# Optimization experiments

Measured on AMD Instinct MI355X. Metric: run time of the kernel, lower is better.

The kernel has to match this reference:

```python
import jax, jax.numpy as jnp
import numpy as np

N = 20000      # nodes
E = 320000     # edges (avg degree 16)
IN, HID, OUT, H = 128, 32, 32, 8
NEG_SLOPE = 0.2


def _gat_conv(x, src, dst, W, al, ar, b):
    """One DGL-style GATConv. x: [N, F_in], W: [F_in, H*D], al/ar: [H, D], b: [H*D].
    Returns [N, H, D]."""
    n = x.shape[0]
    Hh, D = al.shape
    feat = (x @ W).reshape(n, Hh, D)                      # [N,H,D]
    el = jnp.sum(feat * al[None], axis=-1)                # [N,H]
    er = jnp.sum(feat * ar[None], axis=-1)                # [N,H]
    e = jax.nn.leaky_relu(el[src] + er[dst], NEG_SLOPE)   # [E,H]
    # edge softmax over incoming edges of each dst node (stable)
    emax = jax.ops.segment_max(e, dst, num_segments=n)    # [N,H]
    ee = jnp.exp(e - emax[dst])                           # [E,H]
    denom = jax.ops.segment_sum(ee, dst, num_segments=n)  # [N,H]
    alpha = ee / denom[dst]                               # [E,H]
    msg = feat[src] * alpha[:, :, None]                   # [E,H,D] gather+weight
    out = jax.ops.segment_sum(msg, dst, num_segments=n)   # [N,H,D] scatter-add
    return out + b.reshape(1, Hh, D)


def setup_inputs() -> dict:
    key = jax.random.key(0)
    ks = jax.random.split(key, 11)
    return {
        "x":   jax.random.normal(ks[0], (N, IN), dtype=jnp.float32),
        "src": jax.random.randint(ks[1], (E,), 0, N, dtype=jnp.int32),
        "dst": jax.random.randint(ks[2], (E,), 0, N, dtype=jnp.int32),
        "W1":  jax.random.normal(ks[3], (IN, H * HID), dtype=jnp.float32) * 0.1,
        "al1": jax.random.normal(ks[4], (H, HID), dtype=jnp.float32) * 0.1,
        "ar1": jax.random.normal(ks[5], (H, HID), dtype=jnp.float32) * 0.1,
        "b1":  jnp.zeros((H * HID,), dtype=jnp.float32),
        "W2":  jax.random.normal(ks[6], (HID, H * OUT), dtype=jnp.float32) * 0.1,
        "al2": jax.random.normal(ks[7], (H, OUT), dtype=jnp.float32) * 0.1,
        "ar2": jax.random.normal(ks[8], (H, OUT), dtype=jnp.float32) * 0.1,
        "b2":  jnp.zeros((H * OUT,), dtype=jnp.float32),
    }


def reference(x, src, dst, W1, al1, ar1, b1, W2, al2, ar2, b2):
    h = _gat_conv(x, src, dst, W1, al1, ar1, b1)          # [N,H,HID]
    h = jnp.mean(jax.nn.relu(h), axis=1)                  # [N,HID]
    h = _gat_conv(h, src, dst, W2, al2, ar2, b2)          # [N,H,OUT]
    return jnp.mean(h, axis=1)                            # [N,OUT]
```

## Files before the change

kernel.cpp:

```cpp
#include <hip/hip_runtime.h>
#include <hip/hip_bf16.h>

#define N_NODES 20000
#define N_EDGES 320000
#define F_IN    128
#define F_HID   32
#define NHEAD   8
#define FDIM    256
#define CAP     96

typedef __hip_bfloat16 bf16;
typedef __attribute__((ext_vector_type(8))) short short8;
typedef __attribute__((ext_vector_type(4))) float f32x4;

__device__ __forceinline__ unsigned short f2bf_rne(float f){
  unsigned u = __float_as_uint(f);
  unsigned r = u + 0x7FFFu + ((u >> 16) & 1u);
  return (unsigned short)(r >> 16);
}
__device__ __forceinline__ float bf2f(unsigned short s){
  return __uint_as_float((unsigned)s << 16);
}

#define FILLB  ((N_EDGES + 255) / 256)
__global__ void prep_kernel(const int* __restrict__ src, const int* __restrict__ dst,
                            int* __restrict__ cnt, int* __restrict__ bucket,
                            const float* __restrict__ W1, const float* __restrict__ W2,
                            const float* __restrict__ al2, const float* __restrict__ ar2,
                            unsigned short* __restrict__ h1, unsigned short* __restrict__ l1,
                            float* __restrict__ q_lt, float* __restrict__ q_rt){
  const int b = blockIdx.x;
  if (b < FILLB){
    int i = b*256 + threadIdx.x;
    if (i < N_EDGES){
      int d = dst[i];
      int p = atomicAdd(&cnt[d], 1);
      if (p < CAP) bucket[(size_t)d*CAP + p] = src[i];
    }
  } else if (b < FILLB + 128){
    int i = (b - FILLB)*256 + threadIdx.x;
    int n = i >> 7, k = i & 127;
    float v = W1[(size_t)k*FDIM + n];
    unsigned short hs = f2bf_rne(v);
    h1[i] = hs;
    l1[i] = f2bf_rne(v - bf2f(hs));
  } else {
    int t = threadIdx.x;
    int k = t >> 3, hh = t & 7;
    float sl = 0.f, sr = 0.f;
    #pragma unroll
    for (int d = 0; d < 32; d++){
      float w = W2[(size_t)k*FDIM + hh*32 + d];
      sl = fmaf(w, al2[hh*32 + d], sl);
      sr = fmaf(w, ar2[hh*32 + d], sr);
    }
    q_lt[t] = sl;
    q_rt[t] = sr;
  }
}

template<int K>
__global__ __launch_bounds__(256) void gemm_mfma_kernel(
    const float* __restrict__ X,
    const unsigned short* __restrict__ Wthi, const unsigned short* __restrict__ Wtlo,
    const float* __restrict__ al, const float* __restrict__ ar,
    unsigned short* __restrict__ feat, float* __restrict__ el, float* __restrict__ er)
{
  const int tid  = threadIdx.x;
  const int wv   = tid >> 6;
  const int lane = tid & 63;
  const int quad = lane >> 4;
  const int l16  = lane & 15;
  const int m0   = blockIdx.x * 16;
  constexpr int NC = K / 32;

  short8 Ah[NC], Al_[NC];
  {
    const float* xrow = X + (size_t)(m0 + l16)*K;
    #pragma unroll
    for (int c = 0; c < NC; c++){
      float4 a0 = *(const float4*)(xrow + c*32 + quad*8);
      float4 a1 = *(const float4*)(xrow + c*32 + quad*8 + 4);
      const float vs[8] = {a0.x,a0.y,a0.z,a0.w,a1.x,a1.y,a1.z,a1.w};
      #pragma unroll
      for (int j = 0; j < 8; j++){
        unsigned short hs = f2bf_rne(vs[j]);
        Ah[c][j]  = (short)hs;
        Al_[c][j] = (short)f2bf_rne(vs[j] - bf2f(hs));
      }
    }
  }

  float elp[8], erp[8];
  #pragma unroll
  for (int j = 0; j < 8; j++){ elp[j] = 0.f; erp[j] = 0.f; }

  #pragma unroll
  for (int t = 0; t < 4; t++){
    const int nc = wv*64 + t*16;
    const size_t brow = (size_t)(nc + l16) * K;
    f32x4 acc = {0.f, 0.f, 0.f, 0.f};
    #pragma unroll
    for (int c = 0; c < NC; c++){
      short8 Bh = *(const short8*)(Wthi + brow + c*32 + quad*8);
      short8 Bl = *(const short8*)(Wtlo + brow + c*32 + quad*8);
      acc = __builtin_amdgcn_mfma_f32_16x16x32_bf16(Ah[c],  Bh, acc, 0, 0, 0);
      acc = __builtin_amdgcn_mfma_f32_16x16x32_bf16(Ah[c],  Bl, acc, 0, 0, 0);
      acc = __builtin_amdgcn_mfma_f32_16x16x32_bf16(Al_[c], Bh, acc, 0, 0, 0);
    }
    const float alv = al[nc + l16];
    const float arv = ar[nc + l16];
    const int hl = t >> 1;
    #pragma unroll
    for (int r = 0; r < 4; r++){
      float v = acc[r];
      feat[(size_t)(m0 + quad*4 + r)*FDIM + nc + l16] = f2bf_rne(v);
      elp[r*2 + hl] = fmaf(v, alv, elp[r*2 + hl]);
      erp[r*2 + hl] = fmaf(v, arv, erp[r*2 + hl]);
    }
  }

  #pragma unroll
  for (int off = 1; off <= 8; off <<= 1){
    #pragma unroll
    for (int j = 0; j < 8; j++){
      elp[j] += __shfl_xor(elp[j], off);
      erp[j] += __shfl_xor(erp[j], off);
    }
  }
  __shared__ float el_lds[16][8], er_lds[16][8];
  if (l16 == 0){
    #pragma unroll
    for (int r = 0; r < 4; r++){
      #pragma unroll
      for (int hl = 0; hl < 2; hl++){
        el_lds[quad*4 + r][wv*2 + hl] = elp[r*2 + hl];
        er_lds[quad*4 + r][wv*2 + hl] = erp[r*2 + hl];
      }
    }
  }
  __syncthreads();
  if (tid < 128){
    int row = tid >> 3, h = tid & 7;
    el[(size_t)(m0 + row)*NHEAD + h] = el_lds[row][h];
    er[(size_t)(m0 + row)*NHEAD + h] = er_lds[row][h];
  }
}

__global__ __launch_bounds__(256) void edge_agg_l1(
    const bf16* __restrict__ feat, const float* __restrict__ el,
    const float* __restrict__ er, const int* __restrict__ cnt,
    const int* __restrict__ bucket, const float* __restrict__ bias,
    const float* __restrict__ q_lt, const float* __restrict__ q_rt,
    unsigned short* __restrict__ h_out, float* __restrict__ el2,
    float* __restrict__ er2)
{
  const int tid  = threadIdx.x;
  const int wv   = tid >> 6;
  const int lane = tid & 63;
  const int n    = blockIdx.x*4 + wv;

  __shared__ float t_all[4][CAP*9];
  __shared__ int   s_all[4][CAP];
  __shared__ float sum_all[4][NHEAD];
  __shared__ float v_all[4][256];
  float* t_w = t_all[wv];
  int*   s_w = s_all[wv];

  int C = cnt[n];
  if (C > CAP) C = CAP;

  const float4* er4 = (const float4*)(er + (size_t)n*NHEAD);
  float4 era = er4[0], erb = er4[1];
  const float erv[8] = {era.x, era.y, era.z, era.w, erb.x, erb.y, erb.z, erb.w};

  for (int idx = lane; idx < C*2; idx += 64){
    const int e = idx >> 1, j = idx & 1;
    const int sidx = bucket[(size_t)n*CAP + e];
    if (j == 0) s_w[e] = sidx;
    float4 a = ((const float4*)(el + (size_t)sidx*NHEAD))[j];
    const float ev[4] = {a.x, a.y, a.z, a.w};
    #pragma unroll
    for (int hh = 0; hh < 4; hh++){
      float v = ev[hh] + erv[j*4 + hh];
      t_w[e*9 + j*4 + hh] = (v > 0.f) ? v : 0.2f*v;
    }
  }
  {
    const int h = lane >> 3, d = lane & 7;
    float lm = -INFINITY;
    for (int e = d; e < C; e += 8) lm = fmaxf(lm, t_w[e*9 + h]);
    #pragma unroll
    for (int off = 4; off >= 1; off >>= 1) lm = fmaxf(lm, __shfl_xor(lm, off));
    float ls = 0.f;
    for (int e = d; e < C; e += 8){
      float ex = __expf(t_w[e*9 + h] - lm);
      t_w[e*9 + h] = ex;
      ls += ex;
    }
    #pragma unroll
    for (int off = 4; off >= 1; off >>= 1) ls += __shfl_xor(ls, off);
    if (d == 0) sum_all[wv][h] = ls;
  }

  const int sub = lane >> 5;
  const int l   = lane & 31;
  const int hB  = l >> 2;
  const int coff = l << 3;
  float acc[8] = {0,0,0,0,0,0,0,0};
  int e = sub;
  float4 fv;
  if (e < C) fv = *(const float4*)(feat + (size_t)s_w[e]*FDIM + coff);
  while (e < C){
    const int en = e + 2;
    float4 fnext;
    if (en < C) fnext = *(const float4*)(feat + (size_t)s_w[en]*FDIM + coff);
    const float w = t_w[e*9 + hB];
    const unsigned* u = (const unsigned*)&fv;
    #pragma unroll
    for (int j = 0; j < 4; j++){
      float flo = __uint_as_float(u[j] << 16);
      float fhi = __uint_as_float(u[j] & 0xFFFF0000u);
      acc[2*j]   = fmaf(w, flo, acc[2*j]);
      acc[2*j+1] = fmaf(w, fhi, acc[2*j+1]);
    }
    fv = fnext;
    e = en;
  }
  #pragma unroll
  for (int j = 0; j < 8; j++) acc[j] += __shfl_xor(acc[j], 32);

  if (lane < 32){
    const float s = sum_all[wv][l >> 2];
    const float4* b4 = (const float4*)(bias + coff);
    float4 ba = b4[0], bb = b4[1];
    float bv[8] = {ba.x, ba.y, ba.z, ba.w, bb.x, bb.y, bb.z, bb.w};
    float v[8];
    #pragma unroll
    for (int j = 0; j < 8; j++){
      float val = (C > 0) ? (acc[j] / s) : 0.f;
      val += bv[j];
      val = fmaxf(val, 0.f);
      v[j] = val;
    }
    float4* v4 = (float4*)&v_all[wv][coff];
    v4[0] = make_float4(v[0], v[1], v[2], v[3]);
    v4[1] = make_float4(v[4], v[5], v[6], v[7]);
  }
  if (lane < 32){
    float hsum = 0.f;
    #pragma unroll
    for (int hh = 0; hh < 8; hh++) hsum += v_all[wv][hh*32 + lane];
    hsum *= 0.125f;
    h_out[(size_t)n*32 + lane] = f2bf_rne(hsum);

    float4 qa0 = ((const float4*)(q_lt + lane*8))[0];
    float4 qa1 = ((const float4*)(q_lt + lane*8))[1];
    float4 qb0 = ((const float4*)(q_rt + lane*8))[0];
    float4 qb1 = ((const float4*)(q_rt + lane*8))[1];
    float pl[8] = {hsum*qa0.x, hsum*qa0.y, hsum*qa0.z, hsum*qa0.w,
                   hsum*qa1.x, hsum*qa1.y, hsum*qa1.z, hsum*qa1.w};
    float pr[8] = {hsum*qb0.x, hsum*qb0.y, hsum*qb0.z, hsum*qb0.w,
                   hsum*qb1.x, hsum*qb1.y, hsum*qb1.z, hsum*qb1.w};
    #pragma unroll
    for (int off = 1; off <= 16; off <<= 1){
      #pragma unroll
      for (int j = 0; j < 8; j++){
        pl[j] += __shfl_xor(pl[j], off);
        pr[j] += __shfl_xor(pr[j], off);
      }
    }
    if (l == 0){
      #pragma unroll
      for (int j = 0; j < 8; j++){
        el2[(size_t)n*NHEAD + j] = pl[j];
        er2[(size_t)n*NHEAD + j] = pr[j];
      }
    }
  }
}

__global__ __launch_bounds__(256) void edge_agg_l2(
    const unsigned short* __restrict__ h_bf, const float* __restrict__ el2,
    const float* __restrict__ er2, const int* __restrict__ cnt,
    const int* __restrict__ bucket, const float* __restrict__ W2,
    const float* __restrict__ b2, float* __restrict__ outp)
{
  const int tid  = threadIdx.x;
  const int wv   = tid >> 6;
  const int lane = tid & 63;
  const int n    = blockIdx.x*4 + wv;

  __shared__ float t_all[4][CAP*9];
  __shared__ int   s_all[4][CAP];
  __shared__ float sum_all[4][NHEAD];
  __shared__ float A_lds[4][NHEAD][33];
  __shared__ float red[4][256];
  float* t_w = t_all[wv];
  int*   s_w = s_all[wv];

  int C = cnt[n];
  if (C > CAP) C = CAP;

  const float4* er4 = (const float4*)(er2 + (size_t)n*NHEAD);
  float4 era = er4[0], erb = er4[1];
  const float erv[8] = {era.x, era.y, era.z, era.w, erb.x, erb.y, erb.z, erb.w};

  for (int idx = lane; idx < C*2; idx += 64){
    const int e = idx >> 1, j = idx & 1;
    const int sidx = bucket[(size_t)n*CAP + e];
    if (j == 0) s_w[e] = sidx;
    float4 a = ((const float4*)(el2 + (size_t)sidx*NHEAD))[j];
    const float ev[4] = {a.x, a.y, a.z, a.w};
    #pragma unroll
    for (int hh = 0; hh < 4; hh++){
      float v = ev[hh] + erv[j*4 + hh];
      t_w[e*9 + j*4 + hh] = (v > 0.f) ? v : 0.2f*v;
    }
  }
  {
    const int h = lane >> 3, d = lane & 7;
    float lm = -INFINITY;
    for (int e = d; e < C; e += 8) lm = fmaxf(lm, t_w[e*9 + h]);
    #pragma unroll
    for (int off = 4; off >= 1; off >>= 1) lm = fmaxf(lm, __shfl_xor(lm, off));
    float ls = 0.f;
    for (int e = d; e < C; e += 8){
      float ex = __expf(t_w[e*9 + h] - lm);
      t_w[e*9 + h] = ex;
      ls += ex;
    }
    #pragma unroll
    for (int off = 4; off >= 1; off >>= 1) ls += __shfl_xor(ls, off);
    if (d == 0) sum_all[wv][h] = ls;
  }

  const int h  = lane & 7;
  const int dg = lane >> 3;
  float A0=0.f, A1=0.f, A2=0.f, A3=0.f;
  int e = 0;
  ushort4 hv;
  if (e < C) hv = *(const ushort4*)(h_bf + (size_t)s_w[e]*32 + dg*4);
  while (e < C){
    const int en = e + 1;
    ushort4 hnext;
    if (en < C) hnext = *(const ushort4*)(h_bf + (size_t)s_w[en]*32 + dg*4);
    const float w = t_w[e*9 + h];
    A0 = fmaf(w, bf2f(hv.x), A0);
    A1 = fmaf(w, bf2f(hv.y), A1);
    A2 = fmaf(w, bf2f(hv.z), A2);
    A3 = fmaf(w, bf2f(hv.w), A3);
    hv = hnext;
    e = en;
  }
  {
    const float s = sum_all[wv][h];
    const float inv = (C > 0) ? (1.f / s) : 0.f;
    A_lds[wv][h][dg*4 + 0] = A0 * inv;
    A_lds[wv][h][dg*4 + 1] = A1 * inv;
    A_lds[wv][h][dg*4 + 2] = A2 * inv;
    A_lds[wv][h][dg*4 + 3] = A3 * inv;
  }
  __syncthreads();

  {
    const int c  = tid;
    const int hc = c >> 5;
    float p0=0.f, p1=0.f, p2=0.f, p3=0.f;
    for (int k = 0; k < F_HID; k++){
      float w = W2[(size_t)k*FDIM + c];
      p0 = fmaf(A_lds[0][hc][k], w, p0);
      p1 = fmaf(A_lds[1][hc][k], w, p1);
      p2 = fmaf(A_lds[2][hc][k], w, p2);
      p3 = fmaf(A_lds[3][hc][k], w, p3);
    }
    red[0][c] = p0; red[1][c] = p1; red[2][c] = p2; red[3][c] = p3;
  }
  __syncthreads();
  if (tid < 128){
    const int nn = tid >> 5, d = tid & 31;
    float s = 0.f, bm = 0.f;
    #pragma unroll
    for (int hh = 0; hh < 8; hh++){
      s  += red[nn][hh*32 + d];
      bm += b2[hh*32 + d];
    }
    outp[(size_t)(blockIdx.x*4 + nn)*32 + d] = (s + bm) * 0.125f;
  }
}

extern "C" void kernel_launch(void* const* d_in, const int* in_sizes, int n_in,
                              void* d_out, int out_size, void* d_ws, size_t ws_size,
                              hipStream_t stream)
{
  const float* x   = (const float*)d_in[0];
  const int*   src = (const int*)  d_in[1];
  const int*   dst = (const int*)  d_in[2];
  const float* W1  = (const float*)d_in[3];
  const float* al1 = (const float*)d_in[4];
  const float* ar1 = (const float*)d_in[5];
  const float* b1  = (const float*)d_in[6];
  const float* W2  = (const float*)d_in[7];
  const float* al2 = (const float*)d_in[8];
  const float* ar2 = (const float*)d_in[9];
  const float* b2  = (const float*)d_in[10];
  (void)in_sizes; (void)n_in; (void)out_size; (void)ws_size;

  size_t o = 0;
  char* base = (char*)d_ws;
  auto take = [&](size_t bytes) -> char* {
    char* p = base + o;
    o += (bytes + 255) & ~(size_t)255;
    return p;
  };
  unsigned short* feat  = (unsigned short*)take((size_t)N_NODES*FDIM*2);
  float* el1    = (float*)take((size_t)N_NODES*NHEAD*4);
  float* er1    = (float*)take((size_t)N_NODES*NHEAD*4);
  float* el2    = (float*)take((size_t)N_NODES*NHEAD*4);
  float* er2    = (float*)take((size_t)N_NODES*NHEAD*4);
  int*   cnt    = (int*)  take((size_t)N_NODES*4);
  int*   bucket = (int*)  take((size_t)N_NODES*CAP*4);
  unsigned short* hbf  = (unsigned short*)take((size_t)N_NODES*F_HID*2);
  unsigned short* W1th = (unsigned short*)take((size_t)FDIM*F_IN*2);
  unsigned short* W1tl = (unsigned short*)take((size_t)FDIM*F_IN*2);
  float* q_lt   = (float*)take((size_t)F_HID*NHEAD*4);
  float* q_rt   = (float*)take((size_t)F_HID*NHEAD*4);

  hipMemsetAsync(cnt, 0, (size_t)N_NODES*4, stream);
  prep_kernel<<<FILLB + 129, 256, 0, stream>>>(
      src, dst, cnt, bucket, W1, W2, al2, ar2, W1th, W1tl, q_lt, q_rt);

  gemm_mfma_kernel<F_IN><<<N_NODES/16, 256, 0, stream>>>(
      x, W1th, W1tl, al1, ar1, feat, el1, er1);
  edge_agg_l1<<<N_NODES/4, 256, 0, stream>>>(
      (const bf16*)feat, el1, er1, cnt, bucket, b1, q_lt, q_rt, hbf, el2, er2);

  edge_agg_l2<<<N_NODES/4, 256, 0, stream>>>(
      hbf, el2, er2, cnt, bucket, W2, b2, (float*)d_out);
}
```

Before: 196.8 us.

## Fuse edge bucketing into layer-1 GEMM launch and replace memset with init kernel

Replaces the hipMemsetAsync with zeroing of the count array inside the weight-prep kernel. The edge scatter into per-destination buckets moves out of that prep kernel and into the same grid as the layer-1 MFMA GEMM, so the atomic bucketing and the GEMM run concurrently as separate block ranges. This drops one launch and lets the latency-bound atomic scatter overlap the compute-bound GEMM. Scatter blocks returning early inside a kernel with GEMM-sized launch bounds may change scheduling.

```diff
diff --git a/kernel.cpp b/kernel.cpp
--- a/kernel.cpp
+++ b/kernel.cpp
@@ -22,23 +22,18 @@
   return __uint_as_float((unsigned)s << 16);
 }
 
-#define FILLB  ((N_EDGES + 255) / 256)
-__global__ void prep_kernel(const int* __restrict__ src, const int* __restrict__ dst,
-                            int* __restrict__ cnt, int* __restrict__ bucket,
-                            const float* __restrict__ W1, const float* __restrict__ W2,
+#define ZB ((N_NODES + 255) / 256)
+__global__ void init_kernel(const float* __restrict__ W1, const float* __restrict__ W2,
                             const float* __restrict__ al2, const float* __restrict__ ar2,
+                            int* __restrict__ cnt,
                             unsigned short* __restrict__ h1, unsigned short* __restrict__ l1,
                             float* __restrict__ q_lt, float* __restrict__ q_rt){
   const int b = blockIdx.x;
-  if (b < FILLB){
+  if (b < ZB){
     int i = b*256 + threadIdx.x;
-    if (i < N_EDGES){
-      int d = dst[i];
-      int p = atomicAdd(&cnt[d], 1);
-      if (p < CAP) bucket[(size_t)d*CAP + p] = src[i];
-    }
-  } else if (b < FILLB + 128){
-    int i = (b - FILLB)*256 + threadIdx.x;
+    if (i < N_NODES) cnt[i] = 0;
+  } else if (b < ZB + 128){
+    int i = (b - ZB)*256 + threadIdx.x;
     int n = i >> 7, k = i & 127;
     float v = W1[(size_t)k*FDIM + n];
     unsigned short hs = f2bf_rne(v);
@@ -59,19 +54,34 @@
   }
 }
 
-template<int K>
-__global__ __launch_bounds__(256) void gemm_mfma_kernel(
+#define FILLB  ((N_EDGES + 255) / 256)
+#define GEMMB  (N_NODES / 16)
+__global__ __launch_bounds__(256) void scatter_gemm_kernel(
+    const int* __restrict__ src, const int* __restrict__ dst,
+    int* __restrict__ cnt, int* __restrict__ bucket,
     const float* __restrict__ X,
     const unsigned short* __restrict__ Wthi, const unsigned short* __restrict__ Wtlo,
     const float* __restrict__ al, const float* __restrict__ ar,
     unsigned short* __restrict__ feat, float* __restrict__ el, float* __restrict__ er)
 {
+  const int b = blockIdx.x;
+  if (b < FILLB){
+    int i = b*256 + threadIdx.x;
+    if (i < N_EDGES){
+      int d = dst[i];
+      int p = atomicAdd(&cnt[d], 1);
+      if (p < CAP) bucket[(size_t)d*CAP + p] = src[i];
+    }
+    return;
+  }
+
+  constexpr int K = F_IN;
   const int tid  = threadIdx.x;
   const int wv   = tid >> 6;
   const int lane = tid & 63;
   const int quad = lane >> 4;
   const int l16  = lane & 15;
-  const int m0   = blockIdx.x * 16;
+  const int m0   = (b - FILLB) * 16;
   constexpr int NC = K / 32;
 
   short8 Ah[NC], Al_[NC];
@@ -426,12 +436,12 @@
   float* q_lt   = (float*)take((size_t)F_HID*NHEAD*4);
   float* q_rt   = (float*)take((size_t)F_HID*NHEAD*4);
 
-  hipMemsetAsync(cnt, 0, (size_t)N_NODES*4, stream);
-  prep_kernel<<<FILLB + 129, 256, 0, stream>>>(
-      src, dst, cnt, bucket, W1, W2, al2, ar2, W1th, W1tl, q_lt, q_rt);
-
-  gemm_mfma_kernel<F_IN><<<N_NODES/16, 256, 0, stream>>>(
-      x, W1th, W1tl, al1, ar1, feat, el1, er1);
+  init_kernel<<<ZB + 129, 256, 0, stream>>>(
+      W1, W2, al2, ar2, cnt, W1th, W1tl, q_lt, q_rt);
+
+  scatter_gemm_kernel<<<FILLB + GEMMB, 256, 0, stream>>>(
+      src, dst, cnt, bucket, x, W1th, W1tl, al1, ar1, feat, el1, er1);
+
   edge_agg_l1<<<N_NODES/4, 256, 0, stream>>>(
       (const bf16*)feat, el1, er1, cnt, bucket, b1, q_lt, q_rt, hbf, el2, er2);
 
```

New measurement: 193.3 us. Within noise of the previous version (-1.8%).
